# Kernel tuning notes

Measured on AMD Instinct MI355X. Metric: run time of the kernel, lower is better.

The kernel has to match this reference:

```python
import jax, jax.numpy as jnp
import numpy as np

D_MODEL = 768
H = 12
D_K = D_MODEL // H


def setup_inputs() -> dict:
    key = jax.random.key(0)
    ks = jax.random.split(key, 12)
    B, S = 2, 2048
    scale = 1.0 / np.sqrt(D_MODEL)
    q = jax.random.normal(ks[0], (B, S, D_MODEL), jnp.float32)
    k = jax.random.normal(ks[1], (B, S, D_MODEL), jnp.float32)
    v = jax.random.normal(ks[2], (B, S, D_MODEL), jnp.float32)
    mask = jnp.tril(jnp.ones((S, S), jnp.int32))[None, None]  # causal [1,1,S,S]
    wq = jax.random.normal(ks[3], (D_MODEL, D_MODEL), jnp.float32) * scale
    wk = jax.random.normal(ks[4], (D_MODEL, D_MODEL), jnp.float32) * scale
    wv = jax.random.normal(ks[5], (D_MODEL, D_MODEL), jnp.float32) * scale
    wo = jax.random.normal(ks[6], (D_MODEL, D_MODEL), jnp.float32) * scale
    bq = jax.random.normal(ks[7], (D_MODEL,), jnp.float32) * 0.02
    bk = jax.random.normal(ks[8], (D_MODEL,), jnp.float32) * 0.02
    bv = jax.random.normal(ks[9], (D_MODEL,), jnp.float32) * 0.02
    bo = jax.random.normal(ks[10], (D_MODEL,), jnp.float32) * 0.02
    return {"q": q, "k": k, "v": v, "mask": mask,
            "wq": wq, "bq": bq, "wk": wk, "bk": bk,
            "wv": wv, "bv": bv, "wo": wo, "bo": bo}


def reference(q, k, v, mask, wq, bq, wk, bk, wv, bv, wo, bo):
    B, S, _ = q.shape
    # projections (torch Linear: x @ W.T + b)
    qh = (q @ wq.T + bq).reshape(B, S, H, D_K).transpose(0, 2, 1, 3)  # [B,H,S,Dk]
    kh = (k @ wk.T + bk).reshape(B, S, H, D_K).transpose(0, 2, 1, 3)
    vh = (v @ wv.T + bv).reshape(B, S, H, D_K).transpose(0, 2, 1, 3)
    scores = jnp.einsum('bhqd,bhkd->bhqk', qh, kh) / np.sqrt(D_K)
    scores = jnp.where(mask == 0, -jnp.inf, scores)
    attn = jax.nn.softmax(scores, axis=-1)  # dropout p=0.0 (eval) -> identity
    x = jnp.einsum('bhqk,bhkd->bhqd', attn, vh)
    x = x.transpose(0, 2, 1, 3).reshape(B, S, D_MODEL)
    return x @ wo.T + bo
```

## Files before the change

kernel.cpp:

```cpp
#include <hip/hip_runtime.h>
#include <hip/hip_bf16.h>

#define DM 768
#define NH 12
#define DK 64
#define SEQ 2048
#define NB 2
#define M_ (NB*SEQ)
#define XN 3145728
#define WN 589824

typedef __bf16 bf16;
typedef bf16 bf16x2 __attribute__((ext_vector_type(2)));
typedef bf16 bf16x4 __attribute__((ext_vector_type(4)));
typedef bf16 bf16x8 __attribute__((ext_vector_type(8)));
typedef float f32x4 __attribute__((ext_vector_type(4)));
typedef float f32x8 __attribute__((ext_vector_type(8)));

__device__ __forceinline__ f32x4 mfma16(bf16x8 a, bf16x8 b, f32x4 c) {
    return __builtin_amdgcn_mfma_f32_16x16x32_bf16(a, b, c, 0, 0, 0);
}

__device__ __forceinline__ void gload_lds16(const bf16* g, bf16* l) {
    __builtin_amdgcn_global_load_lds(
        (const __attribute__((address_space(1))) void*)g,
        (__attribute__((address_space(3))) void*)l, 16, 0, 0);
}

__device__ __forceinline__ bf16x8 cvt8(f32x8 v) {
    bf16x8 r;
#pragma unroll
    for (int j = 0; j < 8; ++j) r[j] = (bf16)v[j];
    return r;
}

__global__ __launch_bounds__(256) void qkv_gemm_kernel(
    const float* __restrict__ qx, const float* __restrict__ kx, const float* __restrict__ vx,
    const float* __restrict__ wq, const float* __restrict__ wk, const float* __restrict__ wv,
    const float* __restrict__ bq, const float* __restrict__ bk, const float* __restrict__ bv,
    bf16* __restrict__ Qh, bf16* __restrict__ Kh, bf16* __restrict__ Vt)
{
    __shared__ bf16 lds[12288];
    int z = blockIdx.z;
    const float* Xf = (z == 0) ? qx : (z == 1) ? kx : vx;
    const float* Wf = (z == 0) ? wq : (z == 1) ? wk : wv;
    const float* Bi = (z == 0) ? bq : (z == 1) ? bk : bv;

    int t = threadIdx.x;
    int lane = t & 63, w = t >> 6;
    int g = lane >> 4, c = lane & 15;
    int wm = (w >> 1) * 64, wn = (w & 1) * 32;
    int m0 = blockIdx.x * 128, n0 = blockIdx.y * 64;

    f32x4 acc[4][2] = {};

    const float* Agp[4];
    int Al[4];
#pragma unroll
    for (int r = 0; r < 4; ++r) {
        int e = r * 2048 + t * 8;
        int kk = e >> 12, mm = (e & 4095) >> 5, k8 = e & 31;
        Agp[r] = Xf + (size_t)(m0 + mm) * DM + kk * 32 + k8;
        Al[r] = e;
    }
    const float* Bgp[2];
    int Bl[2];
#pragma unroll
    for (int r = 0; r < 2; ++r) {
        int e = r * 2048 + t * 8;
        int kk = e >> 11, nn = (e & 2047) >> 5, k8 = e & 31;
        Bgp[r] = Wf + (size_t)(n0 + nn) * DM + kk * 32 + k8;
        Bl[r] = 8192 + e;
    }

    for (int kt = 0; kt < 12; ++kt) {
        bf16x8 aw[4], bw[2];
#pragma unroll
        for (int r = 0; r < 4; ++r) aw[r] = cvt8(*(const f32x8*)(Agp[r] + kt * 64));
#pragma unroll
        for (int r = 0; r < 2; ++r) bw[r] = cvt8(*(const f32x8*)(Bgp[r] + kt * 64));
#pragma unroll
        for (int r = 0; r < 4; ++r) *(bf16x8*)&lds[Al[r]] = aw[r];
#pragma unroll
        for (int r = 0; r < 2; ++r) *(bf16x8*)&lds[Bl[r]] = bw[r];
        __syncthreads();
        bf16x8 af[4][2], bfr[2][2];
#pragma unroll
        for (int kk = 0; kk < 2; ++kk) {
#pragma unroll
            for (int mi = 0; mi < 4; ++mi)
                af[mi][kk] = *(const bf16x8*)&lds[kk * 4096 + (wm + mi * 16 + c) * 32 + g * 8];
#pragma unroll
            for (int ni = 0; ni < 2; ++ni)
                bfr[ni][kk] = *(const bf16x8*)&lds[8192 + kk * 2048 + (wn + ni * 16 + c) * 32 + g * 8];
        }
#pragma unroll
        for (int mi = 0; mi < 4; ++mi)
#pragma unroll
            for (int ni = 0; ni < 2; ++ni) {
                acc[mi][ni] = mfma16(af[mi][0], bfr[ni][0], acc[mi][ni]);
                acc[mi][ni] = mfma16(af[mi][1], bfr[ni][1], acc[mi][ni]);
            }
        __syncthreads();
    }

    int b_ = m0 >> 11, sbase = m0 & (SEQ - 1);
    int h = blockIdx.y;
    if (z == 0) {
#pragma unroll
        for (int ni = 0; ni < 2; ++ni) {
            int nl = wn + ni * 16 + c;
            float bias = Bi[n0 + nl];
#pragma unroll
            for (int mi = 0; mi < 4; ++mi)
#pragma unroll
                for (int r = 0; r < 4; ++r) {
                    int s = sbase + wm + mi * 16 + g * 4 + r;
                    Qh[((size_t)(b_ * NH + h) * SEQ + s) * DK + nl] = (bf16)(acc[mi][ni][r] + bias);
                }
        }
    } else if (z == 1) {
#pragma unroll
        for (int ni = 0; ni < 2; ++ni) {
            int nl = wn + ni * 16 + c;
            float bias = Bi[n0 + nl];
            int chunk = nl >> 3, e = nl & 7;
#pragma unroll
            for (int mi = 0; mi < 4; ++mi)
#pragma unroll
                for (int r = 0; r < 4; ++r) {
                    int s = sbase + wm + mi * 16 + g * 4 + r;
                    int pos = ((chunk ^ (s & 7)) << 3) + e;
                    Kh[((size_t)(b_ * NH + h) * SEQ + s) * DK + pos] = (bf16)(acc[mi][ni][r] + bias);
                }
        }
    } else {
#pragma unroll
        for (int ni = 0; ni < 2; ++ni) {
            int nl = wn + ni * 16 + c;
            float bias = Bi[n0 + nl];
#pragma unroll
            for (int mi = 0; mi < 4; ++mi) {
                bf16x4 pk;
#pragma unroll
                for (int r = 0; r < 4; ++r) pk[r] = (bf16)(acc[mi][ni][r] + bias);
                int sb = wm + mi * 16;
                int grp64 = sb >> 6, grp = (sb >> 5) & 1, bb = (sb >> 4) & 1;
                int chi = 4 * grp + g;
                int col = grp64 * 64 + ((chi ^ (nl & 7)) << 3) + 4 * bb;
                *(bf16x4*)&lds[nl * 136 + col] = pk;
            }
        }
        __syncthreads();
        int dk = t >> 2, sc = (t & 3) * 32;
        bf16* vdst = Vt + ((size_t)(b_ * NH + h) * DK + dk) * SEQ + sbase + sc;
#pragma unroll
        for (int j = 0; j < 4; ++j)
            *(bf16x8*)(vdst + j * 8) = *(const bf16x8*)&lds[dk * 136 + sc + j * 8];
    }
}

__global__ __launch_bounds__(256) void o_gemm_kernel(
    const bf16* __restrict__ Xo, const float* __restrict__ Wo,
    const float* __restrict__ bo, float* __restrict__ out)
{
    __shared__ bf16 lds[12288];
    int t = threadIdx.x;
    int lane = t & 63, w = t >> 6;
    int g = lane >> 4, c = lane & 15;
    int wm = (w >> 1) * 64, wn = (w & 1) * 32;
    int m0 = blockIdx.x * 128, n0 = blockIdx.y * 64;

    f32x4 acc[4][2] = {};

    const bf16* Agp[4];
#pragma unroll
    for (int r = 0; r < 4; ++r) {
        int e = r * 2048 + t * 8;
        int kk = e >> 12, mm = (e & 4095) >> 5, k8 = e & 31;
        Agp[r] = Xo + (size_t)(m0 + mm) * DM + kk * 32 + k8;
    }
    const float* Bgp[2];
    int Bl[2];
#pragma unroll
    for (int r = 0; r < 2; ++r) {
        int e = r * 2048 + t * 8;
        int kk = e >> 11, nn = (e & 2047) >> 5, k8 = e & 31;
        Bgp[r] = Wo + (size_t)(n0 + nn) * DM + kk * 32 + k8;
        Bl[r] = 8192 + e;
    }

    for (int kt = 0; kt < 12; ++kt) {
#pragma unroll
        for (int r = 0; r < 4; ++r)
            gload_lds16(Agp[r] + kt * 64, &lds[r * 2048 + t * 8]);
        bf16x8 bw[2];
#pragma unroll
        for (int r = 0; r < 2; ++r) bw[r] = cvt8(*(const f32x8*)(Bgp[r] + kt * 64));
#pragma unroll
        for (int r = 0; r < 2; ++r) *(bf16x8*)&lds[Bl[r]] = bw[r];
        __syncthreads();
        bf16x8 af[4][2], bfr[2][2];
#pragma unroll
        for (int kk = 0; kk < 2; ++kk) {
#pragma unroll
            for (int mi = 0; mi < 4; ++mi)
                af[mi][kk] = *(const bf16x8*)&lds[kk * 4096 + (wm + mi * 16 + c) * 32 + g * 8];
#pragma unroll
            for (int ni = 0; ni < 2; ++ni)
                bfr[ni][kk] = *(const bf16x8*)&lds[8192 + kk * 2048 + (wn + ni * 16 + c) * 32 + g * 8];
        }
#pragma unroll
        for (int mi = 0; mi < 4; ++mi)
#pragma unroll
            for (int ni = 0; ni < 2; ++ni) {
                acc[mi][ni] = mfma16(af[mi][0], bfr[ni][0], acc[mi][ni]);
                acc[mi][ni] = mfma16(af[mi][1], bfr[ni][1], acc[mi][ni]);
            }
        __syncthreads();
    }

#pragma unroll
    for (int ni = 0; ni < 2; ++ni) {
        int n = n0 + wn + ni * 16 + c;
        float bias = bo[n];
#pragma unroll
        for (int mi = 0; mi < 4; ++mi)
#pragma unroll
            for (int r = 0; r < 4; ++r)
                out[(size_t)(m0 + wm + mi * 16 + g * 4 + r) * DM + n] = acc[mi][ni][r] + bias;
    }
}

__global__ __launch_bounds__(256) void attn_part_kernel(
    const bf16* __restrict__ Qh, const bf16* __restrict__ Kh, const bf16* __restrict__ Vt,
    bf16* __restrict__ Po, float* __restrict__ Pml)
{
    __shared__ bf16 kt_lds[2][4096];
    __shared__ bf16 vt_lds[2][4096];

    int blk = blockIdx.x;
    int bh = blk % (NB * NH);
    int idx = blk / (NB * NH);
    int J = 31 - (idx >> 1);
    int s = idx & 1;
    int t = threadIdx.x;
    int w = t >> 6, lane = t & 63;
    int g = lane >> 4, c = lane & 15;
    int sw = c & 7;
    const bf16* Qb = Qh + (size_t)bh * SEQ * DK;
    const bf16* Kb = Kh + (size_t)bh * SEQ * DK;
    const bf16* Vb = Vt + (size_t)bh * DK * SEQ;

    const float SCL = 0.125f * 1.4426950408889634f;

    int qa = J * 64 + w * 16;
    int myq = qa + c;
    int nkt = J + 1;
    int tiles0 = (nkt + 1) >> 1;
    int kt_begin = s ? tiles0 : 0;
    int kt_end   = s ? nkt : tiles0;

    float m_st = -INFINITY, l_st = 0.f;
    f32x4 o[4] = {};

    if (kt_begin < kt_end) {
        bf16x8 qf0 = *(const bf16x8*)(Qb + (size_t)(qa + c) * DK + g * 8);
        bf16x8 qf1 = *(const bf16x8*)(Qb + (size_t)(qa + c) * DK + 32 + g * 8);

        auto stage = [&](int kt, int buf) {
            int kb = kt * 64;
            const bf16* kg = Kb + (size_t)kb * DK + t * 8;
#pragma unroll
            for (int i = 0; i < 2; ++i)
                gload_lds16(kg + i * 2048, &kt_lds[buf][i * 2048 + t * 8]);
            int dvr = t >> 3, colc = (t & 7) * 8;
            const bf16* vg = Vb + (size_t)dvr * SEQ + kb + colc;
#pragma unroll
            for (int i = 0; i < 2; ++i)
                gload_lds16(vg + (size_t)(32 * i) * SEQ, &vt_lds[buf][i * 2048 + t * 8]);
        };

        stage(kt_begin, kt_begin & 1);
        for (int kt = kt_begin; kt < kt_end; ++kt) {
            __syncthreads();
            if (kt + 1 < kt_end) stage(kt + 1, (kt + 1) & 1);
            int kb = kt * 64;
            int buf = kt & 1;
            bf16x8 kf[4][2];
#pragma unroll
            for (int i = 0; i < 4; ++i) {
                kf[i][0] = *(const bf16x8*)&kt_lds[buf][(16 * i + c) * 64 + ((g ^ sw) << 3)];
                kf[i][1] = *(const bf16x8*)&kt_lds[buf][(16 * i + c) * 64 + (((4 + g) ^ sw) << 3)];
            }
            bf16x8 vf[2][4];
#pragma unroll
            for (int grp = 0; grp < 2; ++grp)
#pragma unroll
                for (int t2 = 0; t2 < 4; ++t2)
                    vf[grp][t2] = *(const bf16x8*)&vt_lds[buf][(16 * t2 + c) * 64 + (((grp * 4 + g) ^ sw) << 3)];

            bool masked = (kb + 63 > qa);
            float p_[4][4];
#pragma unroll
            for (int i = 0; i < 4; ++i) {
                f32x4 a = {};
                a = mfma16(kf[i][0], qf0, a);
                a = mfma16(kf[i][1], qf1, a);
                if (masked) {
#pragma unroll
                    for (int r = 0; r < 4; ++r) {
                        int key = kb + i * 16 + g * 4 + r;
                        p_[i][r] = (key <= myq) ? a[r] * SCL : -INFINITY;
                    }
                } else {
#pragma unroll
                    for (int r = 0; r < 4; ++r) p_[i][r] = a[r] * SCL;
                }
            }
            float m0_ = fmaxf(fmaxf(p_[0][0], p_[0][1]), fmaxf(p_[0][2], p_[0][3]));
            float m1_ = fmaxf(fmaxf(p_[1][0], p_[1][1]), fmaxf(p_[1][2], p_[1][3]));
            float m2_ = fmaxf(fmaxf(p_[2][0], p_[2][1]), fmaxf(p_[2][2], p_[2][3]));
            float m3_ = fmaxf(fmaxf(p_[3][0], p_[3][1]), fmaxf(p_[3][2], p_[3][3]));
            float mx = fmaxf(fmaxf(m0_, m1_), fmaxf(m2_, m3_));
            mx = fmaxf(mx, __shfl_xor(mx, 16, 64));
            mx = fmaxf(mx, __shfl_xor(mx, 32, 64));
            float m_new = fmaxf(m_st, mx);
            float alpha = exp2f(m_st - m_new);
            m_st = m_new;
#pragma unroll
            for (int i = 0; i < 4; ++i)
#pragma unroll
                for (int r = 0; r < 4; ++r)
                    p_[i][r] = exp2f(p_[i][r] - m_new);
            float s0_ = (p_[0][0] + p_[0][1]) + (p_[0][2] + p_[0][3]);
            float s1_ = (p_[1][0] + p_[1][1]) + (p_[1][2] + p_[1][3]);
            float s2_ = (p_[2][0] + p_[2][1]) + (p_[2][2] + p_[2][3]);
            float s3_ = (p_[3][0] + p_[3][1]) + (p_[3][2] + p_[3][3]);
            float psum = (s0_ + s1_) + (s2_ + s3_);
            psum += __shfl_xor(psum, 16, 64);
            psum += __shfl_xor(psum, 32, 64);
            l_st = l_st * alpha + psum;
#pragma unroll
            for (int t2 = 0; t2 < 4; ++t2)
#pragma unroll
                for (int r = 0; r < 4; ++r) o[t2][r] *= alpha;
            bf16x8 pa0, pa1;
#pragma unroll
            for (int jj = 0; jj < 8; ++jj) {
                pa0[jj] = (bf16)p_[jj >> 2][jj & 3];
                pa1[jj] = (bf16)p_[2 + (jj >> 2)][jj & 3];
            }
#pragma unroll
            for (int t2 = 0; t2 < 4; ++t2) {
                o[t2] = mfma16(vf[0][t2], pa0, o[t2]);
                o[t2] = mfma16(vf[1][t2], pa1, o[t2]);
            }
        }
    }

    size_t base = ((((size_t)bh * 32 + J) * 2 + s) * 64 + w * 16 + c);
    if (g == 0) { Pml[base * 2] = m_st; Pml[base * 2 + 1] = l_st; }
#pragma unroll
    for (int t2 = 0; t2 < 4; ++t2) {
        bf16x4 sa;
#pragma unroll
        for (int r = 0; r < 4; ++r) sa[r] = (bf16)o[t2][r];
        *(bf16x4*)&Po[base * 64 + t2 * 16 + g * 4] = sa;
    }
}

__global__ __launch_bounds__(256) void attn_merge_kernel(
    const bf16* __restrict__ Po, const float* __restrict__ Pml, bf16* __restrict__ Xo)
{
    int idx = blockIdx.x * 256 + threadIdx.x;
    int row = idx >> 2;
    int dq = (idx & 3) * 16;
    int bh = row >> 11;
    int rem = row & 2047;
    int J = rem >> 6, q = rem & 63;
    size_t b0 = (((size_t)bh * 32 + J) * 2 + 0) * 64 + q;
    size_t b1 = b0 + 64;
    float m0 = Pml[b0 * 2], l0 = Pml[b0 * 2 + 1];
    float m1 = Pml[b1 * 2], l1 = Pml[b1 * 2 + 1];
    float mM = fmaxf(m0, m1);
    float sc0 = exp2f(m0 - mM), sc1 = exp2f(m1 - mM);
    float inv = 1.f / (sc0 * l0 + sc1 * l1);
    sc0 *= inv; sc1 *= inv;
    int b_ = bh / NH, h = bh % NH;
    bf16* xrow = Xo + (size_t)(b_ * SEQ + J * 64 + q) * DM + h * DK + dq;
    const bf16* p0 = Po + b0 * 64 + dq;
    const bf16* p1 = Po + b1 * 64 + dq;
    bf16x8 v0a = *(const bf16x8*)p0, v0b = *(const bf16x8*)(p0 + 8);
    bf16x8 v1a = *(const bf16x8*)p1, v1b = *(const bf16x8*)(p1 + 8);
    bf16x8 oa, ob2;
#pragma unroll
    for (int j = 0; j < 8; ++j) {
        oa[j]  = (bf16)(sc0 * (float)v0a[j] + sc1 * (float)v1a[j]);
        ob2[j] = (bf16)(sc0 * (float)v0b[j] + sc1 * (float)v1b[j]);
    }
    *(bf16x8*)xrow = oa;
    *(bf16x8*)(xrow + 8) = ob2;
}

extern "C" void kernel_launch(void* const* d_in, const int* in_sizes, int n_in,
                              void* d_out, int out_size, void* d_ws, size_t ws_size,
                              hipStream_t stream) {
    const float* q  = (const float*)d_in[0];
    const float* k  = (const float*)d_in[1];
    const float* v  = (const float*)d_in[2];
    const float* wq = (const float*)d_in[4];
    const float* bq = (const float*)d_in[5];
    const float* wk = (const float*)d_in[6];
    const float* bk = (const float*)d_in[7];
    const float* wv = (const float*)d_in[8];
    const float* bv = (const float*)d_in[9];
    const float* wo = (const float*)d_in[10];
    const float* bo = (const float*)d_in[11];

    bf16* Xo = (bf16*)d_ws;
    bf16* Qh = Xo + (size_t)XN;
    bf16* Kh = Qh + (size_t)XN;
    bf16* Vt = Kh + (size_t)XN;
    bf16* Po = Vt + (size_t)XN;
    float* Pml = (float*)(Po + 6291456);
    float* out = (float*)d_out;

    dim3 blk(256);
    qkv_gemm_kernel<<<dim3(M_ / 128, DM / 64, 3), blk, 0, stream>>>(
        q, k, v, wq, wk, wv, bq, bk, bv, Qh, Kh, Vt);
    attn_part_kernel<<<dim3(24 * 32 * 2), blk, 0, stream>>>(Qh, Kh, Vt, Po, Pml);
    attn_merge_kernel<<<dim3(768), blk, 0, stream>>>(Po, Pml, Xo);
    o_gemm_kernel<<<dim3(M_ / 128, DM / 64), blk, 0, stream>>>(Xo, wo, bo, out);
}
```

Measured before the change: 216.2 us.

## Prefetch next fp32 tile into registers and XOR-swizzle LDS layout in GEMMs

The QKV and output projection GEMMs now load the next k-tile of fp32 inputs into registers while the current tile is converted and computed, hiding global load latency. LDS writes and reads for the A/B tiles use an XOR swizzle on the 16-byte chunk index to cut bank conflicts in the MFMA fragment reads. The QKV kernel's LDS array grows, and an extra barrier is added before the V epilogue reuses LDS. Register pressure rises from holding the prefetched fp32 vectors.

```diff
diff --git a/kernel.cpp b/kernel.cpp
--- a/kernel.cpp
+++ b/kernel.cpp
@@ -40,7 +40,7 @@
     const float* __restrict__ bq, const float* __restrict__ bk, const float* __restrict__ bv,
     bf16* __restrict__ Qh, bf16* __restrict__ Kh, bf16* __restrict__ Vt)
 {
-    __shared__ bf16 lds[12288];
+    __shared__ bf16 lds[17408];
     int z = blockIdx.z;
     const float* Xf = (z == 0) ? qx : (z == 1) ? kx : vx;
     const float* Wf = (z == 0) ? wq : (z == 1) ? wk : wv;
@@ -61,7 +61,9 @@
         int e = r * 2048 + t * 8;
         int kk = e >> 12, mm = (e & 4095) >> 5, k8 = e & 31;
         Agp[r] = Xf + (size_t)(m0 + mm) * DM + kk * 32 + k8;
-        Al[r] = e;
+        int ch = (e >> 3) & 3;
+        int ch2 = ch ^ (mm & 3) ^ ((mm >> 2) & 3);
+        Al[r] = (e & ~24) | (ch2 << 3);
     }
     const float* Bgp[2];
     int Bl[2];
@@ -70,15 +72,31 @@
         int e = r * 2048 + t * 8;
         int kk = e >> 11, nn = (e & 2047) >> 5, k8 = e & 31;
         Bgp[r] = Wf + (size_t)(n0 + nn) * DM + kk * 32 + k8;
-        Bl[r] = 8192 + e;
-    }
+        int ch = (e >> 3) & 3;
+        int ch2 = ch ^ (nn & 3) ^ ((nn >> 2) & 3);
+        Bl[r] = 8192 + ((e & ~24) | (ch2 << 3));
+    }
+
+    int slot = (g ^ (c & 3) ^ ((c >> 2) & 3)) * 8;
+
+    f32x8 an[4], bn[2];
+#pragma unroll
+    for (int r = 0; r < 4; ++r) an[r] = *(const f32x8*)Agp[r];
+#pragma unroll
+    for (int r = 0; r < 2; ++r) bn[r] = *(const f32x8*)Bgp[r];
 
     for (int kt = 0; kt < 12; ++kt) {
         bf16x8 aw[4], bw[2];
 #pragma unroll
-        for (int r = 0; r < 4; ++r) aw[r] = cvt8(*(const f32x8*)(Agp[r] + kt * 64));
-#pragma unroll
-        for (int r = 0; r < 2; ++r) bw[r] = cvt8(*(const f32x8*)(Bgp[r] + kt * 64));
+        for (int r = 0; r < 4; ++r) aw[r] = cvt8(an[r]);
+#pragma unroll
+        for (int r = 0; r < 2; ++r) bw[r] = cvt8(bn[r]);
+        if (kt < 11) {
+#pragma unroll
+            for (int r = 0; r < 4; ++r) an[r] = *(const f32x8*)(Agp[r] + (kt + 1) * 64);
+#pragma unroll
+            for (int r = 0; r < 2; ++r) bn[r] = *(const f32x8*)(Bgp[r] + (kt + 1) * 64);
+        }
 #pragma unroll
         for (int r = 0; r < 4; ++r) *(bf16x8*)&lds[Al[r]] = aw[r];
 #pragma unroll
@@ -89,10 +107,10 @@
         for (int kk = 0; kk < 2; ++kk) {
 #pragma unroll
             for (int mi = 0; mi < 4; ++mi)
-                af[mi][kk] = *(const bf16x8*)&lds[kk * 4096 + (wm + mi * 16 + c) * 32 + g * 8];
+                af[mi][kk] = *(const bf16x8*)&lds[kk * 4096 + (wm + mi * 16 + c) * 32 + slot];
 #pragma unroll
             for (int ni = 0; ni < 2; ++ni)
-                bfr[ni][kk] = *(const bf16x8*)&lds[8192 + kk * 2048 + (wn + ni * 16 + c) * 32 + g * 8];
+                bfr[ni][kk] = *(const bf16x8*)&lds[8192 + kk * 2048 + (wn + ni * 16 + c) * 32 + slot];
         }
 #pragma unroll
         for (int mi = 0; mi < 4; ++mi)
@@ -135,6 +153,7 @@
                 }
         }
     } else {
+        __syncthreads();
 #pragma unroll
         for (int ni = 0; ni < 2; ++ni) {
             int nl = wn + ni * 16 + c;
@@ -187,8 +206,15 @@
         int e = r * 2048 + t * 8;
         int kk = e >> 11, nn = (e & 2047) >> 5, k8 = e & 31;
         Bgp[r] = Wo + (size_t)(n0 + nn) * DM + kk * 32 + k8;
-        Bl[r] = 8192 + e;
-    }
+        int ch = (e >> 3) & 3;
+        int ch2 = ch ^ (nn & 3) ^ ((nn >> 2) & 3);
+        Bl[r] = 8192 + ((e & ~24) | (ch2 << 3));
+    }
+    int slot = (g ^ (c & 3) ^ ((c >> 2) & 3)) * 8;
+
+    f32x8 bn[2];
+#pragma unroll
+    for (int r = 0; r < 2; ++r) bn[r] = *(const f32x8*)Bgp[r];
 
     for (int kt = 0; kt < 12; ++kt) {
 #pragma unroll
@@ -196,7 +222,11 @@
             gload_lds16(Agp[r] + kt * 64, &lds[r * 2048 + t * 8]);
         bf16x8 bw[2];
 #pragma unroll
-        for (int r = 0; r < 2; ++r) bw[r] = cvt8(*(const f32x8*)(Bgp[r] + kt * 64));
+        for (int r = 0; r < 2; ++r) bw[r] = cvt8(bn[r]);
+        if (kt < 11) {
+#pragma unroll
+            for (int r = 0; r < 2; ++r) bn[r] = *(const f32x8*)(Bgp[r] + (kt + 1) * 64);
+        }
 #pragma unroll
         for (int r = 0; r < 2; ++r) *(bf16x8*)&lds[Bl[r]] = bw[r];
         __syncthreads();
@@ -208,7 +238,7 @@
                 af[mi][kk] = *(const bf16x8*)&lds[kk * 4096 + (wm + mi * 16 + c) * 32 + g * 8];
 #pragma unroll
             for (int ni = 0; ni < 2; ++ni)
-                bfr[ni][kk] = *(const bf16x8*)&lds[8192 + kk * 2048 + (wn + ni * 16 + c) * 32 + g * 8];
+                bfr[ni][kk] = *(const bf16x8*)&lds[8192 + kk * 2048 + (wn + ni * 16 + c) * 32 + slot];
         }
 #pragma unroll
         for (int mi = 0; mi < 4; ++mi)
```

Result: faster. 204.4 us (-5.5%).
